# Performance work log

Hardware: AMD Instinct MI355X
Metric: run time of the kernel (lower is better)

## Reference

```python
import jax, jax.numpy as jnp
import numpy as np
from jax import lax

B, T, D_BERT, H_LSTM, L = 32, 512, 768, 256, 9


def setup_inputs() -> dict:
    key = jax.random.key(0)
    ks = jax.random.split(key, 10)
    def rn(k, shape, s=0.02):
        return jax.random.normal(k, shape, dtype=jnp.float32) * s
    return {
        "seq_out": jax.random.normal(ks[0], (B, T, D_BERT), dtype=jnp.float32),
        "attention_mask": jnp.ones((B, T), dtype=jnp.int32),
        "labels": jax.random.randint(ks[1], (B, T), 0, L),
        "w_ih_f": rn(ks[2], (4 * H_LSTM, D_BERT)),
        "w_hh_f": rn(ks[3], (4 * H_LSTM, H_LSTM)),
        "b_f": jnp.zeros((4 * H_LSTM,), jnp.float32),
        "w_ih_b": rn(ks[4], (4 * H_LSTM, D_BERT)),
        "w_hh_b": rn(ks[5], (4 * H_LSTM, H_LSTM)),
        "b_b": jnp.zeros((4 * H_LSTM,), jnp.float32),
        "w_tag": rn(ks[6], (L, 2 * H_LSTM)),
        "b_tag": jnp.zeros((L,), jnp.float32),
        "start_trans": rn(ks[7], (L,), 0.1),
        "end_trans": rn(ks[8], (L,), 0.1),
        "trans": rn(ks[9], (L, L), 0.1),
    }


def _lstm_dir(x, w_ih, w_hh, b):
    # x: [T, B, D]; torch gate order: i, f, g, o
    Bb, H = x.shape[1], w_hh.shape[1]
    def step(carry, x_t):
        h, c = carry
        g = x_t @ w_ih.T + h @ w_hh.T + b
        i, f, gg, o = jnp.split(g, 4, axis=-1)
        c = jax.nn.sigmoid(f) * c + jax.nn.sigmoid(i) * jnp.tanh(gg)
        h = jax.nn.sigmoid(o) * jnp.tanh(c)
        return (h, c), h
    init = (jnp.zeros((Bb, H), x.dtype), jnp.zeros((Bb, H), x.dtype))
    _, hs = lax.scan(step, init, x)
    return hs  # [T, B, H]


def _emissions(seq_out, w_ih_f, w_hh_f, b_f, w_ih_b, w_hh_b, b_b, w_tag, b_tag):
    x = seq_out.transpose(1, 0, 2)  # [T, B, D]
    hf = _lstm_dir(x, w_ih_f, w_hh_f, b_f)
    hb = _lstm_dir(x[::-1], w_ih_b, w_hh_b, b_b)[::-1]
    h = jnp.concatenate([hf, hb], axis=-1)  # [T, B, 2H] (dropout: eval mode, identity)
    return (h @ w_tag.T + b_tag).transpose(1, 0, 2).astype(jnp.float32)  # [B, T, L]


def _crf_llh(em, tags, mask, start, end, trans):
    # numerator: score of the gold path
    em_sc = jnp.take_along_axis(em, tags[..., None], axis=2)[..., 0]  # [B, T]
    tr_sc = trans[tags[:, :-1], tags[:, 1:]]  # [B, T-1]
    num = start[tags[:, 0]] + em_sc[:, 0] + jnp.sum((tr_sc + em_sc[:, 1:]) * mask[:, 1:], axis=1)
    last_idx = (jnp.sum(mask, axis=1) - 1).astype(jnp.int32)
    last_tags = jnp.take_along_axis(tags, last_idx[:, None], axis=1)[:, 0]
    num = num + end[last_tags]
    # denominator: log-partition via forward algorithm (sequential logsumexp scan)
    def step(score, inp):
        em_t, m_t = inp
        nxt = jax.nn.logsumexp(score[:, :, None] + trans[None] + em_t[:, None, :], axis=1)
        return jnp.where(m_t[:, None] > 0, nxt, score), None
    score0 = start + em[:, 0]
    score, _ = lax.scan(step, score0, (em[:, 1:].transpose(1, 0, 2), mask[:, 1:].T))
    denom = jax.nn.logsumexp(score + end, axis=1)
    return num - denom


def _crf_decode(em, mask, start, end, trans):
    Ll = em.shape[2]
    def step(score, inp):
        em_t, m_t = inp
        comb = score[:, :, None] + trans[None]  # [B, prev, cur]
        nxt = jnp.max(comb, axis=1) + em_t
        bp = jnp.argmax(comb, axis=1)  # [B, L]
        keep = m_t[:, None] > 0
        return jnp.where(keep, nxt, score), jnp.where(keep, bp, jnp.arange(Ll)[None, :])
    score0 = start + em[:, 0]
    final, bps = lax.scan(step, score0, (em[:, 1:].transpose(1, 0, 2), mask[:, 1:].T))
    last = jnp.argmax(final + end, axis=1)  # [B]
    def back(tag, bp_t):
        prev = jnp.take_along_axis(bp_t, tag[:, None], axis=1)[:, 0]
        return prev, prev
    _, earlier = lax.scan(back, last, bps, reverse=True)  # [T-1, B]
    return jnp.concatenate([earlier, last[None]], axis=0).T  # [B, T]


def reference(seq_out, attention_mask, labels, w_ih_f, w_hh_f, b_f, w_ih_b, w_hh_b, b_b, w_tag, b_tag, start_trans, end_trans, trans):
    em = _emissions(seq_out, w_ih_f, w_hh_f, b_f, w_ih_b, w_hh_b, b_b, w_tag, b_tag)
    mask = attention_mask.astype(jnp.float32)
    lbl = jnp.where(labels == -100, 0, labels)
    loss = -jnp.mean(_crf_llh(em, lbl, mask, start_trans, end_trans, trans))
    preds = _crf_decode(em, attention_mask, start_trans, end_trans, trans)
    return em, loss, preds
```

## Files before the change

### kernel.cpp

```cpp
#include <hip/hip_runtime.h>
#include <cmath>


#define NB 32
#define NT 512
#define ND 768
#define NH 256
#define NG 1024
#define NC 2048
#define NL 9
#define NHC 512
#define PPD 32
#define HPAD 260
#define HSZ  (32 * HPAD)
#define NBUF (2 * NB * NH)

typedef float f32x4 __attribute__((ext_vector_type(4)));

static const size_t OFF_WIHT  = 0;
static const size_t OFF_WHHT  = 1572864;
static const size_t OFF_XPART = 2097152;
static const size_t OFF_HCAT  = 35651584;
static const size_t OFF_HG    = 44040192;
static const size_t OFF_CTR   = 44072960;

__global__ void prep(const float* __restrict__ wihf, const float* __restrict__ wihb,
                     const float* __restrict__ whhf, const float* __restrict__ whhb,
                     float* __restrict__ w_ihT, float* __restrict__ w_hhT,
                     float* __restrict__ d_loss, int* __restrict__ flags) {
  int idx = blockIdx.x * 256 + threadIdx.x;
  if (idx == 0) d_loss[0] = 0.f;
  if (idx < 1024) flags[idx] = 0;
  if (idx < 1572864) {
    int k = idx >> 11;
    int c = idx & 2047;
    int d = c >> 10;
    int j = c & 1023;
    w_ihT[idx] = d ? wihb[j * ND + k] : wihf[j * ND + k];
  } else {
    int i2 = idx - 1572864;
    int d = i2 >> 18;
    int r = i2 & 262143;
    int k = r >> 10;
    int j = r & 1023;
    w_hhT[i2] = d ? whhb[j * NH + k] : whhf[j * NH + k];
  }
}

__global__ __launch_bounds__(256, 2)
void gemm_x(const float* __restrict__ x, const float* __restrict__ wT,
            const float* __restrict__ bf, const float* __restrict__ bb,
            float* __restrict__ xpart) {
  __shared__ float As[8][128];
  __shared__ float Bs[8][128];
  const int tid = threadIdx.x;
  const int tx = tid & 15, ty = tid >> 4;
  const int r0 = blockIdx.y * 128, c0 = blockIdx.x * 128;

  float acc[8][8] = {};

  const int arow = tid >> 1;
  const int akq  = (tid & 1) * 4;
  const int rA = r0 + arow;
  const float* aptr = x + ((size_t)((rA & 31) * NT + (rA >> 5)) * ND) + akq;
  const int bk = tid >> 5;
  const int bc = (tid & 31) * 4;
  const float* bptr = wT + (size_t)bk * NC + c0 + bc;

  for (int k0 = 0; k0 < ND; k0 += 8) {
    float4 av = *(const float4*)(aptr + k0);
    float4 bv = *(const float4*)(bptr + (size_t)k0 * NC);
    __syncthreads();
    As[akq + 0][arow] = av.x;
    As[akq + 1][arow] = av.y;
    As[akq + 2][arow] = av.z;
    As[akq + 3][arow] = av.w;
    *(float4*)&Bs[bk][bc] = bv;
    __syncthreads();
#pragma unroll
    for (int k = 0; k < 8; ++k) {
      float4 a0 = *(const float4*)&As[k][ty * 8];
      float4 a1 = *(const float4*)&As[k][ty * 8 + 4];
      float4 b0 = *(const float4*)&Bs[k][tx * 8];
      float4 b1 = *(const float4*)&Bs[k][tx * 8 + 4];
      float am[8] = {a0.x, a0.y, a0.z, a0.w, a1.x, a1.y, a1.z, a1.w};
      float bm[8] = {b0.x, b0.y, b0.z, b0.w, b1.x, b1.y, b1.z, b1.w};
#pragma unroll
      for (int i = 0; i < 8; ++i)
#pragma unroll
        for (int j = 0; j < 8; ++j) acc[i][j] += am[i] * bm[j];
    }
  }

  const int cbase = c0 + tx * 8;
  float bias[8];
#pragma unroll
  for (int j = 0; j < 8; ++j) {
    int c = cbase + j;
    bias[j] = (c < NG) ? bf[c] : bb[c - NG];
  }
#pragma unroll
  for (int i = 0; i < 8; ++i) {
    int r = r0 + ty * 8 + i;
    float4 v0 = {acc[i][0] + bias[0], acc[i][1] + bias[1],
                 acc[i][2] + bias[2], acc[i][3] + bias[3]};
    float4 v1 = {acc[i][4] + bias[4], acc[i][5] + bias[5],
                 acc[i][6] + bias[6], acc[i][7] + bias[7]};
    *(float4*)(xpart + (size_t)r * NC + cbase) = v0;
    *(float4*)(xpart + (size_t)r * NC + cbase + 4) = v1;
  }
}

__global__ __launch_bounds__(512, 1)
void lstm_scan(const float* __restrict__ whhT, const float* __restrict__ xpart,
               float* __restrict__ hcat, float* __restrict__ hG,
               int* __restrict__ flags) {
  __shared__ float wS[2 * 256 * 32];
  __shared__ float hS[2 * HSZ];
  __shared__ float pSw[32 * 68];
  const int tid = threadIdx.x;
  const int m = blockIdx.x;

  for (int dd = 0; dd < 2; ++dd) {
    const float* wsrc = whhT + (size_t)dd * NH * NG;
    for (int it = 0; it < 16; ++it) {
      int i = it * 512 + tid;
      int k = i >> 5, l = i & 31;
      int g = l >> 3, u2 = l & 7;
      wS[(dd * 256 + k) * 32 + l] = wsrc[(size_t)k * NG + g * 256 + m * 8 + u2];
    }
  }
  for (int i = tid; i < 2 * HSZ; i += 512) hS[i] = 0.f;
  __syncthreads();

  const int kh = tid >> 8;
  const int pr = tid & 255;
  const int pb = pr >> 3;
  const int pcg = pr & 7;
  const int l0 = pcg * 4;
  const int ub = tid >> 3;
  const int uu = tid & 7;
  const int c0i = (uu >> 2) * 8 + (uu & 3);

  float cf = 0.f, cb = 0.f;

  for (int s = 0; s < NT; ++s) {
    const int tf = s, tb = NT - 1 - s;

    float xf[4], xb[4];
    if (tid < 256) {
      const float* xpf = xpart + ((size_t)(tf * NB + ub) * NC) + m * 8 + uu;
      const float* xpb = xpart + ((size_t)(tb * NB + ub) * NC) + NG + m * 8 + uu;
#pragma unroll
      for (int g = 0; g < 4; ++g) { xf[g] = xpf[g * 256]; xb[g] = xpb[g * 256]; }
    }

    for (int d = 0; d < 2; ++d) {
      const float* hrow = hS + d * HSZ + pb * HPAD + kh * 128;
      const float* wcol = wS + (size_t)(d * 256 + kh * 128) * 32 + l0;
      f32x4 acc = {0.f, 0.f, 0.f, 0.f};
#pragma unroll 4
      for (int kk = 0; kk < 128; kk += 4) {
        f32x4 hv = *(const f32x4*)(hrow + kk);
        f32x4 w0 = *(const f32x4*)(wcol + (size_t)(kk + 0) * 32);
        f32x4 w1 = *(const f32x4*)(wcol + (size_t)(kk + 1) * 32);
        f32x4 w2 = *(const f32x4*)(wcol + (size_t)(kk + 2) * 32);
        f32x4 w3 = *(const f32x4*)(wcol + (size_t)(kk + 3) * 32);
        acc += hv.x * w0;
        acc += hv.y * w1;
        acc += hv.z * w2;
        acc += hv.w * w3;
      }
      *(f32x4*)(pSw + pb * 68 + (pcg * 2 + kh) * 4) = acc;
      __syncthreads();

      if (tid < 256) {
        const float* pS = pSw + ub * 68;
        const float* xv = d ? xb : xf;
        float g0 = pS[c0i]      + pS[c0i + 4]  + xv[0];
        float g1 = pS[c0i + 16] + pS[c0i + 20] + xv[1];
        float g2 = pS[c0i + 32] + pS[c0i + 36] + xv[2];
        float g3 = pS[c0i + 48] + pS[c0i + 52] + xv[3];
        float ii = 1.f / (1.f + expf(-g0));
        float ff = 1.f / (1.f + expf(-g1));
        float tg = tanhf(g2);
        float oo = 1.f / (1.f + expf(-g3));
        float& cc = d ? cb : cf;
        cc = ff * cc + ii * tg;
        float h = oo * tanhf(cc);
        const int t = d ? tb : tf;
        hcat[((size_t)(ub * NT + t)) * NHC + d * NH + m * 8 + uu] = h;
        float* dst = hG + ((s & 1) ? NBUF : 0) + d * 8192 + m * 256 + ub * 8 + uu;
        __hip_atomic_store(dst, h, __ATOMIC_RELAXED, __HIP_MEMORY_SCOPE_AGENT);
      }
      __syncthreads();
      if (tid == 0)
        __hip_atomic_store(&flags[d * 32 + m], s + 1, __ATOMIC_RELEASE,
                           __HIP_MEMORY_SCOPE_AGENT);
    }

    if (s < NT - 1) {
      const float* bufpar = hG + ((s & 1) ? NBUF : 0);
      for (int d = 0; d < 2; ++d) {
        if (tid < 64) {
          int* fl = flags + d * 32;
          long long t0 = wall_clock64();
          for (;;) {
            int v = (tid < 32)
                ? __hip_atomic_load(&fl[tid], __ATOMIC_RELAXED,
                                    __HIP_MEMORY_SCOPE_AGENT)
                : 0x7fffffff;
            if (__ballot(v > s) == ~0ULL) break;
            if (wall_clock64() - t0 > 200000LL) break;
          }
        }
        __syncthreads();
        const unsigned long long* src = (const unsigned long long*)
            (bufpar + d * 8192);
        unsigned long long vv[8];
#pragma unroll
        for (int i = 0; i < 8; ++i)
          vv[i] = __hip_atomic_load(&src[i * 512 + tid], __ATOMIC_RELAXED,
                                    __HIP_MEMORY_SCOPE_AGENT);
        float* hd = hS + d * HSZ;
#pragma unroll
        for (int i = 0; i < 8; ++i) {
          int f = i * 512 + tid;
          union { unsigned long long uu; float ff2[2]; } cv;
          cv.uu = vv[i];
          int mq = f >> 7;
          int r = f & 127;
          int bb = r >> 2;
          int u2 = (r & 3) * 2;
          hd[bb * HPAD + mq * 8 + u2] = cv.ff2[0];
          hd[bb * HPAD + mq * 8 + u2 + 1] = cv.ff2[1];
        }
        if (d == 0) __syncthreads();
      }
    }
  }
}

__global__ void emissions(const float* __restrict__ hcat, const float* __restrict__ wtag,
                          const float* __restrict__ btag, float* __restrict__ em) {
  __shared__ float wS[NL * NHC];
  const int tid = threadIdx.x;
  for (int i = tid; i < NL * NHC; i += 256) wS[i] = wtag[i];
  __syncthreads();
  const int w = tid >> 6, l = tid & 63;
  const int r = blockIdx.x * 4 + w;
  const float* hp = hcat + (size_t)r * NHC;
  float acc[NL] = {};
#pragma unroll
  for (int rep = 0; rep < 8; ++rep) {
    float hv = hp[l + rep * 64];
#pragma unroll
    for (int j = 0; j < NL; ++j) acc[j] += hv * wS[j * NHC + l + rep * 64];
  }
#pragma unroll
  for (int j = 0; j < NL; ++j) {
#pragma unroll
    for (int off = 32; off; off >>= 1) acc[j] += __shfl_xor(acc[j], off, 64);
  }
  if (l == 0) {
#pragma unroll
    for (int j = 0; j < NL; ++j) em[(size_t)r * NL + j] = acc[j] + btag[j];
  }
}

__global__ void crf_fwd(const float* __restrict__ em, const int* __restrict__ mask,
                        const int* __restrict__ labels, const float* __restrict__ start,
                        const float* __restrict__ endt, const float* __restrict__ trans,
                        float* __restrict__ d_loss) {
  __shared__ float emS[NT * NL];
  __shared__ float maskS[NT];
  __shared__ int lblS[NT];
  const int b = blockIdx.x;
  const int tid = threadIdx.x;
  for (int i = tid; i < NT * NL; i += 64) emS[i] = em[(size_t)b * NT * NL + i];
  for (int i = tid; i < NT; i += 64) {
    maskS[i] = (float)mask[b * NT + i];
    int lb = labels[b * NT + i];
    lblS[i] = (lb == -100) ? 0 : lb;
  }
  __syncthreads();

  float part = 0.f, msum = 0.f;
  for (int t = tid; t < NT; t += 64) {
    msum += maskS[t];
    if (t >= 1)
      part += (trans[lblS[t - 1] * NL + lblS[t]] + emS[t * NL + lblS[t]]) * maskS[t];
  }
#pragma unroll
  for (int off = 32; off; off >>= 1) {
    part += __shfl_xor(part, off, 64);
    msum += __shfl_xor(msum, off, 64);
  }

  const int j = tid >> 2, q = tid & 3;
  const bool leader = (q == 0) && (j < NL);
  float tr0 = 0.f, tr1 = 0.f, tr2 = -1e30f;
  float score = 0.f;
  if (tid < 36) {
    tr0 = trans[q * NL + j];
    tr1 = trans[(q + 4) * NL + j];
    if (q == 0) tr2 = trans[8 * NL + j];
    if (leader) score = start[j] + emS[j];
  }
  for (int t = 1; t < NT; ++t) {
    float s0 = __shfl(score, q * 4, 64);
    float s1 = __shfl(score, (q + 4) * 4, 64);
    float s2 = __shfl(score, 32, 64);
    float v0 = s0 + tr0, v1 = s1 + tr1;
    float v2 = (q == 0) ? (s2 + tr2) : -1e30f;
    float m = fmaxf(fmaxf(v0, v1), v2);
    m = fmaxf(m, __shfl_xor(m, 1, 4));
    m = fmaxf(m, __shfl_xor(m, 2, 4));
    float e = expf(v0 - m) + expf(v1 - m) + ((q == 0) ? expf(v2 - m) : 0.f);
    e += __shfl_xor(e, 1, 4);
    e += __shfl_xor(e, 2, 4);
    if (leader) {
      float nxt = m + logf(e) + emS[t * NL + j];
      score = (maskS[t] > 0.f) ? nxt : score;
    }
  }
  float vs[NL];
  float mx = -1e30f;
#pragma unroll
  for (int jj = 0; jj < NL; ++jj) {
    float sj = __shfl(score, jj * 4, 64) + endt[jj];
    vs[jj] = sj;
    mx = fmaxf(mx, sj);
  }
  float se = 0.f;
#pragma unroll
  for (int jj = 0; jj < NL; ++jj) se += expf(vs[jj] - mx);
  float denom = mx + logf(se);
  if (tid == 0) {
    int li = (int)(msum - 0.5f);
    float num = start[lblS[0]] + emS[lblS[0]] + part + endt[lblS[li]];
    atomicAdd(d_loss, -(num - denom) * (1.f / 32.f));
  }
}

__global__ void crf_viterbi(const float* __restrict__ em, const int* __restrict__ mask,
                            const float* __restrict__ start, const float* __restrict__ endt,
                            const float* __restrict__ trans, float* __restrict__ preds) {
  __shared__ float emS[NT * NL];
  __shared__ int maskS[NT];
  __shared__ short bpS[(NT - 1) * NL];
  __shared__ short tagS[NT];
  const int b = blockIdx.x;
  const int tid = threadIdx.x;
  for (int i = tid; i < NT * NL; i += 64) emS[i] = em[(size_t)b * NT * NL + i];
  for (int i = tid; i < NT; i += 64) maskS[i] = mask[b * NT + i];
  __syncthreads();

  const int j = tid >> 2, q = tid & 3;
  const bool leader = (q == 0) && (j < NL);
  float tr0 = 0.f, tr1 = 0.f, tr2 = -1e30f;
  float score = 0.f;
  if (tid < 36) {
    tr0 = trans[q * NL + j];
    tr1 = trans[(q + 4) * NL + j];
    if (q == 0) tr2 = trans[8 * NL + j];
    if (leader) score = start[j] + emS[j];
  }
  for (int t = 1; t < NT; ++t) {
    float s0 = __shfl(score, q * 4, 64);
    float s1 = __shfl(score, (q + 4) * 4, 64);
    float s2 = __shfl(score, 32, 64);
    float v0 = s0 + tr0, v1 = s1 + tr1;
    float v2 = (q == 0) ? (s2 + tr2) : -1e30f;
    float bv = v0;
    int bi = q;
    if (v1 > bv) { bv = v1; bi = q + 4; }
    if (q == 0 && v2 > bv) { bv = v2; bi = 8; }
#pragma unroll
    for (int off = 1; off <= 2; off <<= 1) {
      float ov = __shfl_xor(bv, off, 4);
      int oi = __shfl_xor(bi, off, 4);
      if (ov > bv || (ov == bv && oi < bi)) { bv = ov; bi = oi; }
    }
    if (leader) {
      int keep = maskS[t];
      float nxt = bv + emS[t * NL + j];
      bpS[(t - 1) * NL + j] = keep ? (short)bi : (short)j;
      score = keep ? nxt : score;
    }
  }
  float fv[NL];
#pragma unroll
  for (int jj = 0; jj < NL; ++jj) fv[jj] = __shfl(score, jj * 4, 64) + endt[jj];
  if (tid == 0) {
    int last = 0;
    float bvv = fv[0];
#pragma unroll
    for (int jj = 1; jj < NL; ++jj)
      if (fv[jj] > bvv) { bvv = fv[jj]; last = jj; }
    tagS[NT - 1] = (short)last;
    for (int t = NT - 1; t >= 1; --t) tagS[t - 1] = bpS[(t - 1) * NL + tagS[t]];
  }
  __syncthreads();
  for (int i = tid; i < NT; i += 64) preds[(size_t)b * NT + i] = (float)tagS[i];
}

extern "C" void kernel_launch(void* const* d_in, const int* in_sizes, int n_in,
                              void* d_out, int out_size, void* d_ws, size_t ws_size,
                              hipStream_t stream) {
  const float* seq_out = (const float*)d_in[0];
  const int* attn = (const int*)d_in[1];
  const int* labels = (const int*)d_in[2];
  const float* w_ih_f = (const float*)d_in[3];
  const float* w_hh_f = (const float*)d_in[4];
  const float* b_f = (const float*)d_in[5];
  const float* w_ih_b = (const float*)d_in[6];
  const float* w_hh_b = (const float*)d_in[7];
  const float* b_b = (const float*)d_in[8];
  const float* w_tag = (const float*)d_in[9];
  const float* b_tag = (const float*)d_in[10];
  const float* start_t = (const float*)d_in[11];
  const float* end_t = (const float*)d_in[12];
  const float* trans = (const float*)d_in[13];
  (void)in_sizes; (void)n_in; (void)out_size; (void)ws_size;

  float* ws = (float*)d_ws;
  float* w_ihT = ws + OFF_WIHT;
  float* w_hhT = ws + OFF_WHHT;
  float* xpart = ws + OFF_XPART;
  float* hcat = ws + OFF_HCAT;
  float* hG = ws + OFF_HG;
  int* flags = (int*)(ws + OFF_CTR);

  float* em = (float*)d_out;
  float* d_loss = em + NB * NT * NL;
  float* preds = d_loss + 1;

  prep<<<8192, 256, 0, stream>>>(w_ih_f, w_ih_b, w_hh_f, w_hh_b, w_ihT, w_hhT, d_loss, flags);
  gemm_x<<<dim3(16, 128), 256, 0, stream>>>(seq_out, w_ihT, b_f, b_b, xpart);
  lstm_scan<<<32, 512, 0, stream>>>(w_hhT, xpart, hcat, hG, flags);
  emissions<<<4096, 256, 0, stream>>>(hcat, w_tag, b_tag, em);
  crf_fwd<<<32, 64, 0, stream>>>(em, attn, labels, start_t, end_t, trans, d_loss);
  crf_viterbi<<<32, 64, 0, stream>>>(em, attn, start_t, end_t, trans, preds);
}
```

Before: 5.851 ms.

## Overlap cross-block hidden-state exchange of one direction with the other direction's gate compute

```diff
diff --git a/kernel.cpp b/kernel.cpp
--- a/kernel.cpp
+++ b/kernel.cpp
@@ -117,7 +117,8 @@
                int* __restrict__ flags) {
   __shared__ float wS[2 * 256 * 32];
   __shared__ float hS[2 * HSZ];
-  __shared__ float pSw[32 * 68];
+  __shared__ float pSwF[32 * 68];
+  __shared__ float pSwB[32 * 68];
   const int tid = threadIdx.x;
   const int m = blockIdx.x;
 
@@ -141,8 +142,13 @@
   const int ub = tid >> 3;
   const int uu = tid & 7;
   const int c0i = (uu >> 2) * 8 + (uu & 3);
+  const int lane = tid & 63;
+  const int uwave = tid >> 6;
 
   float cf = 0.f, cb = 0.f;
+
+  int* flF = flags;
+  int* flB = flags + 128;
 
   for (int s = 0; s < NT; ++s) {
     const int tf = s, tb = NT - 1 - s;
@@ -155,9 +161,9 @@
       for (int g = 0; g < 4; ++g) { xf[g] = xpf[g * 256]; xb[g] = xpb[g * 256]; }
     }
 
-    for (int d = 0; d < 2; ++d) {
-      const float* hrow = hS + d * HSZ + pb * HPAD + kh * 128;
-      const float* wcol = wS + (size_t)(d * 256 + kh * 128) * 32 + l0;
+    {
+      const float* hrow = hS + pb * HPAD + kh * 128;
+      const float* wcol = wS + (size_t)(kh * 128) * 32 + l0;
       f32x4 acc = {0.f, 0.f, 0.f, 0.f};
 #pragma unroll 4
       for (int kk = 0; kk < 128; kk += 4) {
@@ -166,78 +172,128 @@
         f32x4 w1 = *(const f32x4*)(wcol + (size_t)(kk + 1) * 32);
         f32x4 w2 = *(const f32x4*)(wcol + (size_t)(kk + 2) * 32);
         f32x4 w3 = *(const f32x4*)(wcol + (size_t)(kk + 3) * 32);
-        acc += hv.x * w0;
-        acc += hv.y * w1;
-        acc += hv.z * w2;
-        acc += hv.w * w3;
+        acc += hv.x * w0; acc += hv.y * w1; acc += hv.z * w2; acc += hv.w * w3;
       }
-      *(f32x4*)(pSw + pb * 68 + (pcg * 2 + kh) * 4) = acc;
-      __syncthreads();
-
-      if (tid < 256) {
-        const float* pS = pSw + ub * 68;
-        const float* xv = d ? xb : xf;
-        float g0 = pS[c0i]      + pS[c0i + 4]  + xv[0];
-        float g1 = pS[c0i + 16] + pS[c0i + 20] + xv[1];
-        float g2 = pS[c0i + 32] + pS[c0i + 36] + xv[2];
-        float g3 = pS[c0i + 48] + pS[c0i + 52] + xv[3];
-        float ii = 1.f / (1.f + expf(-g0));
-        float ff = 1.f / (1.f + expf(-g1));
-        float tg = tanhf(g2);
-        float oo = 1.f / (1.f + expf(-g3));
-        float& cc = d ? cb : cf;
-        cc = ff * cc + ii * tg;
-        float h = oo * tanhf(cc);
-        const int t = d ? tb : tf;
-        hcat[((size_t)(ub * NT + t)) * NHC + d * NH + m * 8 + uu] = h;
-        float* dst = hG + ((s & 1) ? NBUF : 0) + d * 8192 + m * 256 + ub * 8 + uu;
-        __hip_atomic_store(dst, h, __ATOMIC_RELAXED, __HIP_MEMORY_SCOPE_AGENT);
+      *(f32x4*)(pSwF + pb * 68 + (pcg * 2 + kh) * 4) = acc;
+    }
+    __syncthreads();
+
+    if (tid < 256) {
+      const float* pS = pSwF + ub * 68;
+      float g0 = pS[c0i]      + pS[c0i + 4]  + xf[0];
+      float g1 = pS[c0i + 16] + pS[c0i + 20] + xf[1];
+      float g2 = pS[c0i + 32] + pS[c0i + 36] + xf[2];
+      float g3 = pS[c0i + 48] + pS[c0i + 52] + xf[3];
+      float ii = 1.f / (1.f + expf(-g0));
+      float ff = 1.f / (1.f + expf(-g1));
+      float tg = tanhf(g2);
+      float oo = 1.f / (1.f + expf(-g3));
+      cf = ff * cf + ii * tg;
+      float h = oo * tanhf(cf);
+      hcat[((size_t)(ub * NT + tf)) * NHC + m * 8 + uu] = h;
+      float* dst = hG + ((s & 1) ? NBUF : 0) + m * 256 + ub * 8 + uu;
+      __hip_atomic_store(dst, h, __ATOMIC_RELAXED, __HIP_MEMORY_SCOPE_AGENT);
+      if (lane == 0)
+        __hip_atomic_store(&flF[m * 4 + uwave], s + 1, __ATOMIC_RELEASE,
+                           __HIP_MEMORY_SCOPE_AGENT);
+    } else if (s > 0) {
+      {
+        const long long* fl2 = (const long long*)flB;
+        long long t0 = wall_clock64();
+        for (;;) {
+          long long v = __hip_atomic_load(&fl2[lane], __ATOMIC_RELAXED,
+                                          __HIP_MEMORY_SCOPE_AGENT);
+          int lo = (int)v, hi = (int)(v >> 32);
+          if (__ballot(lo >= s && hi >= s) == ~0ULL) break;
+          if (wall_clock64() - t0 > 200000LL) break;
+        }
       }
-      __syncthreads();
-      if (tid == 0)
-        __hip_atomic_store(&flags[d * 32 + m], s + 1, __ATOMIC_RELEASE,
+      const unsigned long long* src = (const unsigned long long*)
+          (hG + (((s - 1) & 1) ? NBUF : 0) + 8192);
+      unsigned long long vv[16];
+#pragma unroll
+      for (int i = 0; i < 16; ++i)
+        vv[i] = __hip_atomic_load(&src[i * 256 + (tid - 256)], __ATOMIC_RELAXED,
+                                  __HIP_MEMORY_SCOPE_AGENT);
+      float* hd = hS + HSZ;
+#pragma unroll
+      for (int i = 0; i < 16; ++i) {
+        int f = i * 256 + (tid - 256);
+        union { unsigned long long uu; float ff2[2]; } cv;
+        cv.uu = vv[i];
+        int mq = f >> 7, r = f & 127, bb = r >> 2, u2 = (r & 3) * 2;
+        hd[bb * HPAD + mq * 8 + u2] = cv.ff2[0];
+        hd[bb * HPAD + mq * 8 + u2 + 1] = cv.ff2[1];
+      }
+    }
+    __syncthreads();
+
+    {
+      const float* hrow = hS + HSZ + pb * HPAD + kh * 128;
+      const float* wcol = wS + (size_t)(256 + kh * 128) * 32 + l0;
+      f32x4 acc = {0.f, 0.f, 0.f, 0.f};
+#pragma unroll 4
+      for (int kk = 0; kk < 128; kk += 4) {
+        f32x4 hv = *(const f32x4*)(hrow + kk);
+        f32x4 w0 = *(const f32x4*)(wcol + (size_t)(kk + 0) * 32);
+        f32x4 w1 = *(const f32x4*)(wcol + (size_t)(kk + 1) * 32);
+        f32x4 w2 = *(const f32x4*)(wcol + (size_t)(kk + 2) * 32);
+        f32x4 w3 = *(const f32x4*)(wcol + (size_t)(kk + 3) * 32);
+        acc += hv.x * w0; acc += hv.y * w1; acc += hv.z * w2; acc += hv.w * w3;
+      }
+      *(f32x4*)(pSwB + pb * 68 + (pcg * 2 + kh) * 4) = acc;
+    }
+    __syncthreads();
+
+    if (tid < 256) {
+      const float* pS = pSwB + ub * 68;
+      float g0 = pS[c0i]      + pS[c0i + 4]  + xb[0];
+      float g1 = pS[c0i + 16] + pS[c0i + 20] + xb[1];
+      float g2 = pS[c0i + 32] + pS[c0i + 36] + xb[2];
+      float g3 = pS[c0i + 48] + pS[c0i + 52] + xb[3];
+      float ii = 1.f / (1.f + expf(-g0));
+      float ff = 1.f / (1.f + expf(-g1));
+      float tg = tanhf(g2);
+      float oo = 1.f / (1.f + expf(-g3));
+      cb = ff * cb + ii * tg;
+      float h = oo * tanhf(cb);
+      hcat[((size_t)(ub * NT + tb)) * NHC + NH + m * 8 + uu] = h;
+      float* dst = hG + ((s & 1) ? NBUF : 0) + 8192 + m * 256 + ub * 8 + uu;
+      __hip_atomic_store(dst, h, __ATOMIC_RELAXED, __HIP_MEMORY_SCOPE_AGENT);
+      if (lane == 0)
+        __hip_atomic_store(&flB[m * 4 + uwave], s + 1, __ATOMIC_RELEASE,
                            __HIP_MEMORY_SCOPE_AGENT);
-    }
-
-    if (s < NT - 1) {
-      const float* bufpar = hG + ((s & 1) ? NBUF : 0);
-      for (int d = 0; d < 2; ++d) {
-        if (tid < 64) {
-          int* fl = flags + d * 32;
-          long long t0 = wall_clock64();
-          for (;;) {
-            int v = (tid < 32)
-                ? __hip_atomic_load(&fl[tid], __ATOMIC_RELAXED,
-                                    __HIP_MEMORY_SCOPE_AGENT)
-                : 0x7fffffff;
-            if (__ballot(v > s) == ~0ULL) break;
-            if (wall_clock64() - t0 > 200000LL) break;
-          }
+    } else if (s < NT - 1) {
+      {
+        const long long* fl2 = (const long long*)flF;
+        long long t0 = wall_clock64();
+        for (;;) {
+          long long v = __hip_atomic_load(&fl2[lane], __ATOMIC_RELAXED,
+                                          __HIP_MEMORY_SCOPE_AGENT);
+          int lo = (int)v, hi = (int)(v >> 32);
+          if (__ballot(lo >= s + 1 && hi >= s + 1) == ~0ULL) break;
+          if (wall_clock64() - t0 > 200000LL) break;
         }
-        __syncthreads();
-        const unsigned long long* src = (const unsigned long long*)
-            (bufpar + d * 8192);
-        unsigned long long vv[8];
-#pragma unroll
-        for (int i = 0; i < 8; ++i)
-          vv[i] = __hip_atomic_load(&src[i * 512 + tid], __ATOMIC_RELAXED,
-                                    __HIP_MEMORY_SCOPE_AGENT);
-        float* hd = hS + d * HSZ;
-#pragma unroll
-        for (int i = 0; i < 8; ++i) {
-          int f = i * 512 + tid;
-          union { unsigned long long uu; float ff2[2]; } cv;
-          cv.uu = vv[i];
-          int mq = f >> 7;
-          int r = f & 127;
-          int bb = r >> 2;
-          int u2 = (r & 3) * 2;
-          hd[bb * HPAD + mq * 8 + u2] = cv.ff2[0];
-          hd[bb * HPAD + mq * 8 + u2 + 1] = cv.ff2[1];
-        }
-        if (d == 0) __syncthreads();
       }
-    }
+      const unsigned long long* src = (const unsigned long long*)
+          (hG + ((s & 1) ? NBUF : 0));
+      unsigned long long vv[16];
+#pragma unroll
+      for (int i = 0; i < 16; ++i)
+        vv[i] = __hip_atomic_load(&src[i * 256 + (tid - 256)], __ATOMIC_RELAXED,
+                                  __HIP_MEMORY_SCOPE_AGENT);
+      float* hd = hS;
+#pragma unroll
+      for (int i = 0; i < 16; ++i) {
+        int f = i * 256 + (tid - 256);
+        union { unsigned long long uu; float ff2[2]; } cv;
+        cv.uu = vv[i];
+        int mq = f >> 7, r = f & 127, bb = r >> 2, u2 = (r & 3) * 2;
+        hd[bb * HPAD + mq * 8 + u2] = cv.ff2[0];
+        hd[bb * HPAD + mq * 8 + u2 + 1] = cv.ff2[1];
+      }
+    }
+    __syncthreads();
   }
 }
 
```

Result: slower. 6.833 ms (+16.8%).
